# Kernel tuning notes

Measured on AMD Instinct MI355X. Metric: run time of the kernel, lower is better.

## Reference

```python
import jax, jax.numpy as jnp
import numpy as np

N_NODES = 50000
N_EDGES = 800000
D_FEAT = 96
HOP_NUM = 4


def setup_inputs() -> dict:
    key = jax.random.key(0)
    k1, k2, k3, k4, k5 = jax.random.split(key, 5)
    h = jax.random.normal(k1, (N_NODES, D_FEAT), dtype=jnp.float32)
    # per-node degree-normalization scalar (ndata['d']), e.g. deg^{-1/2}
    d = jax.random.uniform(k2, (N_NODES,), dtype=jnp.float32)
    src = jax.random.randint(k3, (N_EDGES,), 0, N_NODES)
    dst = jax.random.randint(k4, (N_EDGES,), 0, N_NODES)
    # layerRegular: hop_num learned scalars, init U[0,1)
    layer_regular = jax.random.uniform(k5, (HOP_NUM,), dtype=jnp.float32)
    return {"h": h, "d": d, "src": src, "dst": dst, "layer_regular": layer_regular}


def reference(h, d, src, dst, layer_regular):
    # edge weights: e = d_dst * d_src  (edge_applying with m == 1)
    e = (d[dst] * d[src])[:, None]  # [E, 1]

    def spmm(x):
        # update_all(u_mul_e('h','e'), sum): gather src feats, scale, scatter-add to dst
        return jax.ops.segment_sum(x[src] * e, dst, num_segments=N_NODES)

    feat = h
    hops = []
    for i in range(HOP_NUM):
        r = layer_regular[i]
        feat = spmm(feat) * r + (1.0 - r) * feat  # residual blend
        # feature_drop with p=0.0 is identity
        hops.append(feat)
    return jnp.concatenate(hops, axis=1)  # [N, hop_num * D]
```

## Files before the change

kernel.cpp:

```cpp
#include <hip/hip_runtime.h>

#define N_NODES 50000
#define N_EDGES 800000
#define D_FEAT 96
#define HOP_NUM 4
#define OUT_STRIDE (HOP_NUM * D_FEAT)
#define SCAN_B 256
#define NBLK_SCAN ((N_NODES + SCAN_B - 1) / SCAN_B)
#define EB_BLOCKS ((N_EDGES + 255) / 256)
#define F2B_VEC (N_NODES * D_FEAT / 4)

#define GROUP 24
#define GPB 8
#define HOP_BLOCK (GROUP * GPB)

typedef float f32x4 __attribute__((ext_vector_type(4)));

__device__ __forceinline__ unsigned short f2bf(float x) {
    union { float f; unsigned u; } c; c.f = x;
    unsigned r = (c.u + 0x7FFFu + ((c.u >> 16) & 1u)) >> 16;
    return (unsigned short)r;
}
__device__ __forceinline__ float bf2f(unsigned short b) {
    union { unsigned u; float f; } c; c.u = ((unsigned)b) << 16;
    return c.f;
}


__global__ void zero_deg_kernel(int* __restrict__ deg) {
    int i = blockIdx.x * blockDim.x + threadIdx.x;
    if (i < N_NODES) deg[i] = 0;
}

__global__ void hist_kernel(const int* __restrict__ dst, int* __restrict__ deg) {
    int e = blockIdx.x * blockDim.x + threadIdx.x;
    if (e >= N_EDGES) return;
    atomicAdd(&deg[dst[e]], 1);
}

__global__ void scanA_kernel(const int* __restrict__ deg, int* __restrict__ off,
                             int* __restrict__ partials) {
    int i = blockIdx.x * SCAN_B + threadIdx.x;
    int v = (i < N_NODES) ? deg[i] : 0;
    int lane = threadIdx.x & 63;
    int wid  = threadIdx.x >> 6;
    int x = v;
    #pragma unroll
    for (int o = 1; o < 64; o <<= 1) {
        int y = __shfl_up(x, o, 64);
        if (lane >= o) x += y;
    }
    __shared__ int wtot[SCAN_B / 64];
    if (lane == 63) wtot[wid] = x;
    __syncthreads();
    int wbase = 0;
    #pragma unroll
    for (int w = 0; w < SCAN_B / 64; ++w) wbase += (w < wid) ? wtot[w] : 0;
    if (i < N_NODES) off[i] = wbase + x - v;
    if (threadIdx.x == SCAN_B - 1) partials[blockIdx.x] = wbase + x;
}

__global__ void scanB_kernel(int* __restrict__ partials) {
    int tid = threadIdx.x;
    int v = (tid < NBLK_SCAN) ? partials[tid] : 0;
    int lane = tid & 63;
    int wid  = tid >> 6;
    int x = v;
    #pragma unroll
    for (int o = 1; o < 64; o <<= 1) {
        int y = __shfl_up(x, o, 64);
        if (lane >= o) x += y;
    }
    __shared__ int wtot[SCAN_B / 64];
    if (lane == 63) wtot[wid] = x;
    __syncthreads();
    int wbase = 0;
    #pragma unroll
    for (int w = 0; w < SCAN_B / 64; ++w) wbase += (w < wid) ? wtot[w] : 0;
    if (tid < NBLK_SCAN) partials[tid] = wbase + x - v;
}

__global__ void scanC_kernel(int* __restrict__ off, const int* __restrict__ partials,
                             int* __restrict__ cursor) {
    int i = blockIdx.x * SCAN_B + threadIdx.x;
    if (i < N_NODES) {
        off[i] += partials[blockIdx.x];
        cursor[i] = 0;
    }
    if (i == 0) off[N_NODES] = N_EDGES;
}

__global__ void scatter_kernel(const int* __restrict__ src, const int* __restrict__ dst,
                               const int* __restrict__ off, int* __restrict__ cursor,
                               int* __restrict__ ssrc) {
    int e = blockIdx.x * blockDim.x + threadIdx.x;
    if (e >= N_EDGES) return;
    int t = dst[e];
    int s = src[e];
    int p = atomicAdd(&cursor[t], 1);
    ssrc[off[t] + p] = s;
}

__global__ void f32_to_bf16_kernel(const float* __restrict__ in, unsigned short* __restrict__ out) {
    int i = blockIdx.x * blockDim.x + threadIdx.x;
    if (i >= F2B_VEC) return;
    float4 v = ((const float4*)in)[i];
    ushort4 o;
    o.x = f2bf(v.x); o.y = f2bf(v.y); o.z = f2bf(v.z); o.w = f2bf(v.w);
    ((ushort4*)out)[i] = o;
}

__global__ void __launch_bounds__(HOP_BLOCK)
spmm_gather_kernel(const unsigned short* __restrict__ tab,
                   const int* __restrict__ off,
                   const int* __restrict__ ssrc,
                   const float* __restrict__ dn,
                   const float* __restrict__ lr, int hop,
                   float* __restrict__ out,
                   unsigned short* __restrict__ tab_next) {
    int t = blockIdx.x * HOP_BLOCK + threadIdx.x;
    int gid = t / GROUP;
    int lane = t % GROUP;
    if (gid >= N_NODES) return;
    int beg = off[gid];
    int end = off[gid + 1];
    float dnt = dn[gid];

    float4 acc = make_float4(0.f, 0.f, 0.f, 0.f);
    int k = beg;
    for (; k + 4 <= end; k += 4) {
        int s0 = ssrc[k];
        int s1 = ssrc[k + 1];
        int s2 = ssrc[k + 2];
        int s3 = ssrc[k + 3];
        float w0 = dn[s0] * dnt;
        float w1 = dn[s1] * dnt;
        float w2 = dn[s2] * dnt;
        float w3 = dn[s3] * dnt;
        ushort4 u0 = ((const ushort4*)(tab + (long long)s0 * D_FEAT))[lane];
        ushort4 u1 = ((const ushort4*)(tab + (long long)s1 * D_FEAT))[lane];
        ushort4 u2 = ((const ushort4*)(tab + (long long)s2 * D_FEAT))[lane];
        ushort4 u3 = ((const ushort4*)(tab + (long long)s3 * D_FEAT))[lane];
        acc.x = fmaf(bf2f(u0.x), w0, fmaf(bf2f(u1.x), w1, fmaf(bf2f(u2.x), w2, fmaf(bf2f(u3.x), w3, acc.x))));
        acc.y = fmaf(bf2f(u0.y), w0, fmaf(bf2f(u1.y), w1, fmaf(bf2f(u2.y), w2, fmaf(bf2f(u3.y), w3, acc.y))));
        acc.z = fmaf(bf2f(u0.z), w0, fmaf(bf2f(u1.z), w1, fmaf(bf2f(u2.z), w2, fmaf(bf2f(u3.z), w3, acc.z))));
        acc.w = fmaf(bf2f(u0.w), w0, fmaf(bf2f(u1.w), w1, fmaf(bf2f(u2.w), w2, fmaf(bf2f(u3.w), w3, acc.w))));
    }
    for (; k < end; ++k) {
        int s = ssrc[k];
        float w = dn[s] * dnt;
        ushort4 u = ((const ushort4*)(tab + (long long)s * D_FEAT))[lane];
        acc.x = fmaf(bf2f(u.x), w, acc.x);
        acc.y = fmaf(bf2f(u.y), w, acc.y);
        acc.z = fmaf(bf2f(u.z), w, acc.z);
        acc.w = fmaf(bf2f(u.w), w, acc.w);
    }

    float r = lr[hop];
    ushort4 pu = ((const ushort4*)(tab + (long long)gid * D_FEAT))[lane];
    f32x4 o;
    o.x = acc.x * r + (1.0f - r) * bf2f(pu.x);
    o.y = acc.y * r + (1.0f - r) * bf2f(pu.y);
    o.z = acc.z * r + (1.0f - r) * bf2f(pu.z);
    o.w = acc.w * r + (1.0f - r) * bf2f(pu.w);
    __builtin_nontemporal_store(o, (f32x4*)(out + (long long)gid * OUT_STRIDE) + lane);
    if (tab_next) {
        ushort4 ov;
        ov.x = f2bf(o.x); ov.y = f2bf(o.y); ov.z = f2bf(o.z); ov.w = f2bf(o.w);
        ((ushort4*)(tab_next + (long long)gid * D_FEAT))[lane] = ov;
    }
}

extern "C" void kernel_launch(void* const* d_in, const int* in_sizes, int n_in,
                              void* d_out, int out_size, void* d_ws, size_t ws_size,
                              hipStream_t stream) {
    const float* h   = (const float*)d_in[0];
    const float* dn  = (const float*)d_in[1];
    const int*   src = (const int*)d_in[2];
    const int*   dst = (const int*)d_in[3];
    const float* lr  = (const float*)d_in[4];
    float* out = (float*)d_out;

    char* base = (char*)d_ws;
    unsigned short* tabA = (unsigned short*)base; base += (size_t)N_NODES * D_FEAT * sizeof(unsigned short);
    unsigned short* tabB = (unsigned short*)base; base += (size_t)N_NODES * D_FEAT * sizeof(unsigned short);
    int* ssrc     = (int*)base;                   base += (size_t)N_EDGES * sizeof(int);
    int* off      = (int*)base;                   base += (N_NODES + 1) * sizeof(int);
    int* deg      = (int*)base;                   base += N_NODES * sizeof(int);
    int* cursor   = (int*)base;                   base += N_NODES * sizeof(int);
    int* partials = (int*)base;                   base += NBLK_SCAN * sizeof(int);

    zero_deg_kernel<<<NBLK_SCAN, SCAN_B, 0, stream>>>(deg);
    hist_kernel<<<EB_BLOCKS, 256, 0, stream>>>(dst, deg);
    scanA_kernel<<<NBLK_SCAN, SCAN_B, 0, stream>>>(deg, off, partials);
    scanB_kernel<<<1, SCAN_B, 0, stream>>>(partials);
    scanC_kernel<<<NBLK_SCAN, SCAN_B, 0, stream>>>(off, partials, cursor);
    scatter_kernel<<<EB_BLOCKS, 256, 0, stream>>>(src, dst, off, cursor, ssrc);
    f32_to_bf16_kernel<<<(F2B_VEC + 255) / 256, 256, 0, stream>>>(h, tabA);

    const int HB = (N_NODES + GPB - 1) / GPB;
    unsigned short* cur = tabA;
    unsigned short* nxt = tabB;
    for (int hop = 0; hop < HOP_NUM; ++hop) {
        unsigned short* wr = (hop == HOP_NUM - 1) ? (unsigned short*)nullptr : nxt;
        spmm_gather_kernel<<<HB, HOP_BLOCK, 0, stream>>>(cur, off, ssrc, dn, lr, hop,
                                                         out + hop * D_FEAT, wr);
        unsigned short* t = cur; cur = nxt; nxt = t;
    }
}
```

Before: 220.6 us.

## Remap SpMM hop kernel to one thread per node per feature quarter

Replaces the 24-lane-per-node gather kernel with a kernel where each thread owns one destination node and a quarter of the 96 features, walking its whole edge list alone. The grid is interleaved so the four feature quarters of a node block are scheduled next to each other, with the intent of sharing source rows in cache. The edge-index reads become nontemporal loads. In exchange, neighbouring lanes now read different rows (48-byte chunks), so gathers and output stores are much less coalesced. Lanes in a wavefront also diverge on node degree.

New measurement: 747.4 us. +238.8%, slower.

```diff
diff --git a/kernel.cpp b/kernel.cpp
--- a/kernel.cpp
+++ b/kernel.cpp
@@ -10,9 +10,11 @@
 #define EB_BLOCKS ((N_EDGES + 255) / 256)
 #define F2B_VEC (N_NODES * D_FEAT / 4)
 
-#define GROUP 24
-#define GPB 8
-#define HOP_BLOCK (GROUP * GPB)
+#define SPLIT 4
+#define CH_Q (D_FEAT / SPLIT)
+#define U4_Q (CH_Q / 4)
+#define NODE_BLOCKS ((N_NODES + 255) / 256)
+#define HOP_GRID (NODE_BLOCKS / 2 * 8)
 
 typedef float f32x4 __attribute__((ext_vector_type(4)));
 
@@ -110,64 +112,58 @@
     ((ushort4*)out)[i] = o;
 }
 
-__global__ void __launch_bounds__(HOP_BLOCK)
-spmm_gather_kernel(const unsigned short* __restrict__ tab,
-                   const int* __restrict__ off,
-                   const int* __restrict__ ssrc,
-                   const float* __restrict__ dn,
-                   const float* __restrict__ lr, int hop,
-                   float* __restrict__ out,
-                   unsigned short* __restrict__ tab_next) {
-    int t = blockIdx.x * HOP_BLOCK + threadIdx.x;
-    int gid = t / GROUP;
-    int lane = t % GROUP;
-    if (gid >= N_NODES) return;
-    int beg = off[gid];
-    int end = off[gid + 1];
-    float dnt = dn[gid];
-
-    float4 acc = make_float4(0.f, 0.f, 0.f, 0.f);
-    int k = beg;
-    for (; k + 4 <= end; k += 4) {
-        int s0 = ssrc[k];
-        int s1 = ssrc[k + 1];
-        int s2 = ssrc[k + 2];
-        int s3 = ssrc[k + 3];
-        float w0 = dn[s0] * dnt;
-        float w1 = dn[s1] * dnt;
-        float w2 = dn[s2] * dnt;
-        float w3 = dn[s3] * dnt;
-        ushort4 u0 = ((const ushort4*)(tab + (long long)s0 * D_FEAT))[lane];
-        ushort4 u1 = ((const ushort4*)(tab + (long long)s1 * D_FEAT))[lane];
-        ushort4 u2 = ((const ushort4*)(tab + (long long)s2 * D_FEAT))[lane];
-        ushort4 u3 = ((const ushort4*)(tab + (long long)s3 * D_FEAT))[lane];
-        acc.x = fmaf(bf2f(u0.x), w0, fmaf(bf2f(u1.x), w1, fmaf(bf2f(u2.x), w2, fmaf(bf2f(u3.x), w3, acc.x))));
-        acc.y = fmaf(bf2f(u0.y), w0, fmaf(bf2f(u1.y), w1, fmaf(bf2f(u2.y), w2, fmaf(bf2f(u3.y), w3, acc.y))));
-        acc.z = fmaf(bf2f(u0.z), w0, fmaf(bf2f(u1.z), w1, fmaf(bf2f(u2.z), w2, fmaf(bf2f(u3.z), w3, acc.z))));
-        acc.w = fmaf(bf2f(u0.w), w0, fmaf(bf2f(u1.w), w1, fmaf(bf2f(u2.w), w2, fmaf(bf2f(u3.w), w3, acc.w))));
-    }
-    for (; k < end; ++k) {
-        int s = ssrc[k];
+__global__ void __launch_bounds__(256)
+spmm_hop_kernel(const unsigned short* __restrict__ tab,
+                const int* __restrict__ off,
+                const int* __restrict__ ssrc,
+                const float* __restrict__ dn,
+                const float* __restrict__ lr, int hop,
+                float* __restrict__ out,
+                unsigned short* __restrict__ tab_next) {
+    int q  = (blockIdx.x & 7) >> 1;
+    int nb = ((blockIdx.x >> 3) << 1) | (blockIdx.x & 1);
+    int n  = nb * 256 + threadIdx.x;
+    if (n >= N_NODES) return;
+    int beg = off[n];
+    int end = off[n + 1];
+    float dnt = dn[n];
+
+    float acc[CH_Q];
+    #pragma unroll
+    for (int c = 0; c < CH_Q; ++c) acc[c] = 0.f;
+
+    for (int k = beg; k < end; ++k) {
+        int s = __builtin_nontemporal_load(&ssrc[k]);
         float w = dn[s] * dnt;
-        ushort4 u = ((const ushort4*)(tab + (long long)s * D_FEAT))[lane];
-        acc.x = fmaf(bf2f(u.x), w, acc.x);
-        acc.y = fmaf(bf2f(u.y), w, acc.y);
-        acc.z = fmaf(bf2f(u.z), w, acc.z);
-        acc.w = fmaf(bf2f(u.w), w, acc.w);
+        const ushort4* r4 = (const ushort4*)(tab + (size_t)s * D_FEAT) + q * U4_Q;
+        #pragma unroll
+        for (int c = 0; c < U4_Q; ++c) {
+            ushort4 u = r4[c];
+            acc[4 * c + 0] = fmaf(bf2f(u.x), w, acc[4 * c + 0]);
+            acc[4 * c + 1] = fmaf(bf2f(u.y), w, acc[4 * c + 1]);
+            acc[4 * c + 2] = fmaf(bf2f(u.z), w, acc[4 * c + 2]);
+            acc[4 * c + 3] = fmaf(bf2f(u.w), w, acc[4 * c + 3]);
+        }
     }
 
     float r = lr[hop];
-    ushort4 pu = ((const ushort4*)(tab + (long long)gid * D_FEAT))[lane];
-    f32x4 o;
-    o.x = acc.x * r + (1.0f - r) * bf2f(pu.x);
-    o.y = acc.y * r + (1.0f - r) * bf2f(pu.y);
-    o.z = acc.z * r + (1.0f - r) * bf2f(pu.z);
-    o.w = acc.w * r + (1.0f - r) * bf2f(pu.w);
-    __builtin_nontemporal_store(o, (f32x4*)(out + (long long)gid * OUT_STRIDE) + lane);
-    if (tab_next) {
-        ushort4 ov;
-        ov.x = f2bf(o.x); ov.y = f2bf(o.y); ov.z = f2bf(o.z); ov.w = f2bf(o.w);
-        ((ushort4*)(tab_next + (long long)gid * D_FEAT))[lane] = ov;
+    const ushort4* prow = (const ushort4*)(tab + (size_t)n * D_FEAT) + q * U4_Q;
+    f32x4* orow = (f32x4*)(out + (size_t)n * OUT_STRIDE) + q * U4_Q;
+    ushort4* trow = tab_next ? ((ushort4*)(tab_next + (size_t)n * D_FEAT) + q * U4_Q) : nullptr;
+    #pragma unroll
+    for (int c = 0; c < U4_Q; ++c) {
+        ushort4 pu = prow[c];
+        f32x4 o;
+        o.x = acc[4 * c + 0] * r + (1.0f - r) * bf2f(pu.x);
+        o.y = acc[4 * c + 1] * r + (1.0f - r) * bf2f(pu.y);
+        o.z = acc[4 * c + 2] * r + (1.0f - r) * bf2f(pu.z);
+        o.w = acc[4 * c + 3] * r + (1.0f - r) * bf2f(pu.w);
+        __builtin_nontemporal_store(o, orow + c);
+        if (trow) {
+            ushort4 ov;
+            ov.x = f2bf(o.x); ov.y = f2bf(o.y); ov.z = f2bf(o.z); ov.w = f2bf(o.w);
+            trow[c] = ov;
+        }
     }
 }
 
@@ -198,13 +194,12 @@
     scatter_kernel<<<EB_BLOCKS, 256, 0, stream>>>(src, dst, off, cursor, ssrc);
     f32_to_bf16_kernel<<<(F2B_VEC + 255) / 256, 256, 0, stream>>>(h, tabA);
 
-    const int HB = (N_NODES + GPB - 1) / GPB;
     unsigned short* cur = tabA;
     unsigned short* nxt = tabB;
     for (int hop = 0; hop < HOP_NUM; ++hop) {
         unsigned short* wr = (hop == HOP_NUM - 1) ? (unsigned short*)nullptr : nxt;
-        spmm_gather_kernel<<<HB, HOP_BLOCK, 0, stream>>>(cur, off, ssrc, dn, lr, hop,
-                                                         out + hop * D_FEAT, wr);
+        spmm_hop_kernel<<<HOP_GRID, 256, 0, stream>>>(cur, off, ssrc, dn, lr, hop,
+                                                      out + hop * D_FEAT, wr);
         unsigned short* t = cur; cur = nxt; nxt = t;
     }
 }
```
